# Kernel tuning notes

Measured on AMD Instinct MI355X. Metric: run time of the kernel, lower is better.

Reference implementation:

```python
import jax, jax.numpy as jnp
import numpy as np

HEADS = 8
DIM_HEAD = 64
NB_FEATURES = 256
DIM = 512

def setup_inputs() -> dict:
    key = jax.random.key(0)
    ks = jax.random.split(key, 4)
    b, n = 2, 8192
    x = jax.random.normal(ks[0], (b, n, DIM), jnp.float32)
    # fan-in scaling so exp(feature projections) stays numerically sane
    Wqkv = jax.random.normal(ks[1], (3 * HEADS * DIM_HEAD, DIM), jnp.float32) / np.sqrt(DIM).astype(np.float32)
    Wout = jax.random.normal(ks[2], (DIM, HEADS * DIM_HEAD), jnp.float32) / np.sqrt(HEADS * DIM_HEAD).astype(np.float32)
    bout = jnp.zeros((DIM,), jnp.float32)
    proj = jax.random.normal(ks[3], (NB_FEATURES, DIM_HEAD), jnp.float32) / np.sqrt(DIM_HEAD).astype(np.float32)
    return {"x": x, "Wqkv": Wqkv, "Wout": Wout, "bout": bout, "proj": proj}

def reference(x, Wqkv, Wout, bout, proj):
    b, n, _ = x.shape
    scale = DIM_HEAD ** -0.5
    qkv = jnp.einsum('bnd,ed->bne', x, Wqkv)            # [b,n,3*h*dh]
    q, k, v = jnp.split(qkv, 3, axis=-1)
    to_heads = lambda t: t.reshape(b, n, HEADS, DIM_HEAD).transpose(0, 2, 1, 3)  # [b,h,n,dh]
    q = to_heads(q) * scale
    k = to_heads(k)
    v = to_heads(v)
    # FAVOR+ exp feature maps
    q_prime = jnp.exp(jnp.einsum('bhnd,fd->bhnf', q, proj))  # [b,h,n,f]
    k_prime = jnp.exp(jnp.einsum('bhnd,fd->bhnf', k, proj))  # [b,h,n,f]
    k_sum = k_prime.sum(axis=2)                              # [b,h,f]
    D = jnp.einsum('bhnf,bhf->bhn', q_prime, k_sum)          # normalizer
    D_inv = 1.0 / (D + 1e-6)
    context = jnp.einsum('bhmf,bhmd->bhfd', k_prime, v)      # [b,h,f,dh]
    out = jnp.einsum('bhnf,bhfd->bhnd', q_prime, context) * D_inv[..., None]
    out = out.transpose(0, 2, 1, 3).reshape(b, n, HEADS * DIM_HEAD)
    return jnp.einsum('bne,de->bnd', out, Wout) + bout
```

## Files before the change

### kernel.cpp

```cpp
#include <hip/hip_runtime.h>
#include <math.h>

#define B_    2
#define NSEQ  8192
#define DIM_  512
#define H_    8
#define DH_   64
#define F_    256
#define M_    (B_*NSEQ)
#define QKV_  1536

typedef __attribute__((ext_vector_type(8))) short     short8;
typedef __attribute__((ext_vector_type(4))) float     float4v;
typedef __attribute__((ext_vector_type(8))) unsigned short ushort8v;

__device__ __forceinline__ unsigned short f2bf(float f) {
    unsigned u = __float_as_uint(f);
    u += 0x7FFFu + ((u >> 16) & 1u);
    return (unsigned short)(u >> 16);
}
__device__ __forceinline__ unsigned pack2bf(float lo, float hi) {
    return __builtin_amdgcn_perm(__float_as_uint(hi), __float_as_uint(lo), 0x07060302);
}
__device__ __forceinline__ void glds16(const void* g, void* s) {
    __builtin_amdgcn_global_load_lds(
        (const __attribute__((address_space(1))) unsigned int*)g,
        (__attribute__((address_space(3))) unsigned int*)s, 16, 0, 0);
}

__global__ __launch_bounds__(256) void cvt_bf16(const float* __restrict__ in,
                                                unsigned short* __restrict__ out,
                                                int n8) {
    int i = blockIdx.x * 256 + threadIdx.x;
    if (i >= n8) return;
    float4 a = ((const float4*)in)[2 * i];
    float4 b = ((const float4*)in)[2 * i + 1];
    ushort8v o;
    o[0] = f2bf(a.x); o[1] = f2bf(a.y); o[2] = f2bf(a.z); o[3] = f2bf(a.w);
    o[4] = f2bf(b.x); o[5] = f2bf(b.y); o[6] = f2bf(b.z); o[7] = f2bf(b.w);
    ((ushort8v*)out)[i] = o;
}

template<bool BF16OUT>
__global__ __launch_bounds__(256) void gemm_nt_mfma(const unsigned short* __restrict__ A,
                                                    const unsigned short* __restrict__ Bm,
                                                    const float* __restrict__ bias,
                                                    void* __restrict__ Cout,
                                                    int M, int N, int K) {
    __shared__ __align__(16) unsigned short As[128 * 32];
    __shared__ __align__(16) unsigned short Bs[128 * 32];
    const int t  = threadIdx.x;
    const int w  = t >> 6, l = t & 63;
    const int wm = w >> 1, wn = w & 1;
    const int m0 = blockIdx.y * 128, n0 = blockIdx.x * 128;
    const int lrow = l & 15, lkb = l >> 4;

    float4v acc[4][4];
#pragma unroll
    for (int mi = 0; mi < 4; mi++)
#pragma unroll
        for (int ni = 0; ni < 4; ni++) acc[mi][ni] = (float4v){0.f, 0.f, 0.f, 0.f};

    for (int k0 = 0; k0 < K; k0 += 32) {
        __syncthreads();
#pragma unroll
        for (int i = 0; i < 2; i++) {
            int rb8 = w * 2 + i;
            int row = rb8 * 16 + lrow;
            glds16(A + (size_t)(m0 + row) * K + k0 + lkb * 8, &As[rb8 * 512]);
            glds16(Bm + (size_t)(n0 + row) * K + k0 + lkb * 8, &Bs[rb8 * 512]);
        }
        __syncthreads();

        short8 af[4], bfr[4];
#pragma unroll
        for (int mi = 0; mi < 4; mi++)
            af[mi] = *(const short8*)&As[((wm * 4 + mi) * 64 + l) * 8];
#pragma unroll
        for (int ni = 0; ni < 4; ni++)
            bfr[ni] = *(const short8*)&Bs[((wn * 4 + ni) * 64 + l) * 8];
#pragma unroll
        for (int mi = 0; mi < 4; mi++)
#pragma unroll
            for (int ni = 0; ni < 4; ni++)
                acc[mi][ni] = __builtin_amdgcn_mfma_f32_16x16x32_bf16(
                    af[mi], bfr[ni], acc[mi][ni], 0, 0, 0);
    }

    const int q = l >> 4, c = l & 15;
#pragma unroll
    for (int mi = 0; mi < 4; mi++) {
        int row0 = m0 + wm * 64 + mi * 16 + q * 4;
#pragma unroll
        for (int ni = 0; ni < 4; ni++) {
            int col = n0 + wn * 64 + ni * 16 + c;
            float bv = bias ? bias[col] : 0.f;
#pragma unroll
            for (int r = 0; r < 4; r++) {
                float v = acc[mi][ni][r] + bv;
                if (BF16OUT) ((unsigned short*)Cout)[(size_t)(row0 + r) * N + col] = f2bf(v);
                else         ((float*)Cout)[(size_t)(row0 + r) * N + col] = v;
            }
        }
    }
}

__global__ __launch_bounds__(256) void vtrans(const unsigned short* __restrict__ qkvb,
                                              unsigned short* __restrict__ vT) {
    __shared__ unsigned short T[128][80];
    const int t = threadIdx.x;
    const int n0 = blockIdx.x * 128, z = blockIdx.y;
    const int b = z >> 3, h = z & 7;
#pragma unroll
    for (int i = 0; i < 4; i++) {
        int flat = t + i * 256;
        int n = flat >> 3, d8 = flat & 7;
        ushort8v v = *(const ushort8v*)(qkvb + ((size_t)b * NSEQ + n0 + n) * QKV_ + 1024 + h * 64 + d8 * 8);
        *(ushort8v*)&T[n][d8 * 8] = v;
    }
    __syncthreads();
#pragma unroll
    for (int i = 0; i < 4; i++) {
        int flat = t + i * 256;
        int d = flat >> 4, n8 = flat & 15;
        ushort8v o;
#pragma unroll
        for (int j = 0; j < 8; j++) o[j] = T[n8 * 8 + j][d];
        *(ushort8v*)(vT + ((size_t)z * 64 + d) * NSEQ + n0 + n8 * 8) = o;
    }
}

__global__ __launch_bounds__(256) void ctx_fused_mfma(
    const unsigned short* __restrict__ qkvb,
    const unsigned short* __restrict__ projb,
    const unsigned short* __restrict__ vT,
    float* __restrict__ partial)
{
    __shared__ __align__(16) unsigned short PB[32 * 512];
    __shared__ __align__(16) unsigned short KB[8 * 512];
    __shared__ __align__(16) unsigned short VB[8 * 512];
    __shared__ __align__(16) unsigned short KPA[32 * 512];
    const int t = threadIdx.x, w = t >> 6, l = t & 63;
    const int lr = l & 15, lq = l >> 4;
    const int s = blockIdx.x, z = blockIdx.y;
    const int b = z >> 3, h = z & 7;
    const int nchunk = s * 256;

    for (int idx = w; idx < 32; idx += 4) {
        int fblk = idx >> 1, kt = idx & 1;
        glds16(projb + (size_t)(fblk * 16 + lr) * 64 + kt * 32 + lq * 8, &PB[idx * 512]);
    }

    float4v acc[4][5];
#pragma unroll
    for (int mi = 0; mi < 4; mi++)
#pragma unroll
        for (int ni = 0; ni < 5; ni++) acc[mi][ni] = (float4v){0.f, 0.f, 0.f, 0.f};
    short ov = (lr == 0) ? (short)0x3F80 : (short)0;
    short8 ones = {ov, ov, ov, ov, ov, ov, ov, ov};

    for (int st = 0; st < 4; st++) {
        int nbase = nchunk + st * 64;
        __syncthreads();
        for (int idx = w; idx < 8; idx += 4) {
            int nblk = idx >> 1, kt = idx & 1;
            glds16(qkvb + ((size_t)b * NSEQ + nbase + nblk * 16 + lr) * QKV_ + 512 + h * 64 + kt * 32 + lq * 8,
                   &KB[idx * 512]);
        }
        for (int idx = w; idx < 8; idx += 4) {
            int dhb = idx >> 1, nt2 = idx & 1;
            glds16(vT + ((size_t)z * 64 + dhb * 16 + lr) * NSEQ + nbase + nt2 * 32 + lq * 8,
                   &VB[idx * 512]);
        }
        __syncthreads();

        float4v a2[4][4];
#pragma unroll
        for (int mi = 0; mi < 4; mi++)
#pragma unroll
            for (int ni = 0; ni < 4; ni++) a2[mi][ni] = (float4v){0.f, 0.f, 0.f, 0.f};
#pragma unroll
        for (int ks = 0; ks < 2; ks++) {
            short8 ka[4], pb[4];
#pragma unroll
            for (int mi = 0; mi < 4; mi++)
                ka[mi] = *(const short8*)&KB[((mi * 2 + ks) * 64 + l) * 8];
#pragma unroll
            for (int ni = 0; ni < 4; ni++)
                pb[ni] = *(const short8*)&PB[(((w * 4 + ni) * 2 + ks) * 64 + l) * 8];
#pragma unroll
            for (int mi = 0; mi < 4; mi++)
#pragma unroll
                for (int ni = 0; ni < 4; ni++)
                    a2[mi][ni] = __builtin_amdgcn_mfma_f32_16x16x32_bf16(ka[mi], pb[ni], a2[mi][ni], 0, 0, 0);
        }
#pragma unroll
        for (int mi = 0; mi < 4; mi++) {
            int nb = mi * 16 + lq * 4;
            int qoff = ((nb >> 3) & 3) * 256 + (nb & 7) * 2;
            int setn = nb >> 5;
#pragma unroll
            for (int ni = 0; ni < 4; ni++) {
                int f = w * 64 + ni * 16 + lr;
                float e0 = __expf(a2[mi][ni][0]);
                float e1 = __expf(a2[mi][ni][1]);
                float e2 = __expf(a2[mi][ni][2]);
                float e3 = __expf(a2[mi][ni][3]);
                uint2 p; p.x = pack2bf(e0, e1); p.y = pack2bf(e2, e3);
                *(uint2*)((char*)KPA + (size_t)(((f >> 4) * 2 + setn) * 1024 + qoff + (f & 15) * 16)) = p;
            }
        }
#pragma unroll
        for (int ks = 0; ks < 2; ks++) {
            short8 af[4], bf[4];
#pragma unroll
            for (int mi = 0; mi < 4; mi++)
                af[mi] = *(const short8*)&KPA[(((w * 4 + mi) * 2 + ks) * 64 + l) * 8];
#pragma unroll
            for (int ni = 0; ni < 4; ni++)
                bf[ni] = *(const short8*)&VB[((ni * 2 + ks) * 64 + l) * 8];
#pragma unroll
            for (int mi = 0; mi < 4; mi++) {
#pragma unroll
                for (int ni = 0; ni < 4; ni++)
                    acc[mi][ni] = __builtin_amdgcn_mfma_f32_16x16x32_bf16(af[mi], bf[ni], acc[mi][ni], 0, 0, 0);
                acc[mi][4] = __builtin_amdgcn_mfma_f32_16x16x32_bf16(af[mi], ones, acc[mi][4], 0, 0, 0);
            }
        }
    }
    float* base = partial + (size_t)(s * 16 + z) * 80 * 256;
#pragma unroll
    for (int mi = 0; mi < 4; mi++) {
        int f0r = w * 64 + mi * 16 + lq * 4;
#pragma unroll
        for (int ni = 0; ni < 5; ni++) {
            int col = ni * 16 + lr;
#pragma unroll
            for (int r = 0; r < 4; r++)
                base[(size_t)col * 256 + f0r + r] = acc[mi][ni][r];
        }
    }
}

__global__ __launch_bounds__(256) void ctx_reduce(const float* __restrict__ partial,
                                                  unsigned short* __restrict__ ctxT) {
    int idx = blockIdx.x * 256 + threadIdx.x;
    const int NC = 16 * 80 * 256;
    if (idx >= NC) return;
    float s = 0.f;
#pragma unroll
    for (int k = 0; k < 32; k++) s += partial[(size_t)k * NC + idx];
    ctxT[idx] = f2bf(s);
}

__global__ __launch_bounds__(256) void attn_fused_mfma(
    const unsigned short* __restrict__ qkvb,
    const unsigned short* __restrict__ projb,
    const unsigned short* __restrict__ ctxT,
    unsigned short* __restrict__ attnb)
{
    __shared__ __align__(16) unsigned short QB[16 * 512];
    __shared__ __align__(16) unsigned short PA[8 * 512];
    __shared__ __align__(16) unsigned short QPA[16 * 512];
    __shared__ __align__(16) unsigned short CB[10 * 512];
    const int t = threadIdx.x, w = t >> 6, l = t & 63;
    const int lr = l & 15, lq = l >> 4;
    const int m0 = blockIdx.x * 128, z = blockIdx.y;
    const int b = z >> 3, h = z & 7;

    for (int idx = w; idx < 16; idx += 4) {
        int mblk = idx >> 1, kt = idx & 1;
        glds16(qkvb + ((size_t)b * NSEQ + m0 + mblk * 16 + lr) * QKV_ + h * 64 + kt * 32 + lq * 8,
               &QB[idx * 512]);
    }
    float4v acc[2][5];
#pragma unroll
    for (int mi = 0; mi < 2; mi++)
#pragma unroll
        for (int ni = 0; ni < 5; ni++) acc[mi][ni] = (float4v){0.f, 0.f, 0.f, 0.f};

    for (int fs = 0; fs < 4; fs++) {
        int f0 = fs * 64;
        __syncthreads();
        for (int idx = w; idx < 8; idx += 4) {
            int fb = idx >> 1, kt = idx & 1;
            glds16(projb + (size_t)(f0 + fb * 16 + lr) * 64 + kt * 32 + lq * 8, &PA[idx * 512]);
        }
        for (int idx = w; idx < 10; idx += 4) {
            int dhb = idx >> 1, ft = idx & 1;
            glds16(ctxT + ((size_t)z * 80 + dhb * 16 + lr) * 256 + f0 + ft * 32 + lq * 8,
                   &CB[idx * 512]);
        }
        __syncthreads();

        float4v a2[4][2];
#pragma unroll
        for (int mi = 0; mi < 4; mi++)
#pragma unroll
            for (int ni = 0; ni < 2; ni++) a2[mi][ni] = (float4v){0.f, 0.f, 0.f, 0.f};
#pragma unroll
        for (int ks = 0; ks < 2; ks++) {
            short8 pa[4], qb[2];
#pragma unroll
            for (int mi = 0; mi < 4; mi++)
                pa[mi] = *(const short8*)&PA[((mi * 2 + ks) * 64 + l) * 8];
#pragma unroll
            for (int ni = 0; ni < 2; ni++)
                qb[ni] = *(const short8*)&QB[(((w * 2 + ni) * 2 + ks) * 64 + l) * 8];
#pragma unroll
            for (int mi = 0; mi < 4; mi++)
#pragma unroll
                for (int ni = 0; ni < 2; ni++)
                    a2[mi][ni] = __builtin_amdgcn_mfma_f32_16x16x32_bf16(pa[mi], qb[ni], a2[mi][ni], 0, 0, 0);
        }
#pragma unroll
        for (int mi = 0; mi < 4; mi++) {
            int fb2 = mi * 16 + lq * 4;
            int qoff = ((fb2 >> 3) & 3) * 256 + (fb2 & 7) * 2;
            int setf = fb2 >> 5;
#pragma unroll
            for (int ni = 0; ni < 2; ni++) {
                int m = w * 32 + ni * 16 + lr;
                float e0 = __expf(0.125f * a2[mi][ni][0]);
                float e1 = __expf(0.125f * a2[mi][ni][1]);
                float e2 = __expf(0.125f * a2[mi][ni][2]);
                float e3 = __expf(0.125f * a2[mi][ni][3]);
                uint2 p; p.x = pack2bf(e0, e1); p.y = pack2bf(e2, e3);
                *(uint2*)((char*)QPA + (size_t)(((m >> 4) * 2 + setf) * 1024 + qoff + (m & 15) * 16)) = p;
            }
        }
#pragma unroll
        for (int ks = 0; ks < 2; ks++) {
            short8 af[2], cb[5];
#pragma unroll
            for (int mi = 0; mi < 2; mi++)
                af[mi] = *(const short8*)&QPA[(((w * 2 + mi) * 2 + ks) * 64 + l) * 8];
#pragma unroll
            for (int ni = 0; ni < 5; ni++)
                cb[ni] = *(const short8*)&CB[((ni * 2 + ks) * 64 + l) * 8];
#pragma unroll
            for (int mi = 0; mi < 2; mi++)
#pragma unroll
                for (int ni = 0; ni < 5; ni++)
                    acc[mi][ni] = __builtin_amdgcn_mfma_f32_16x16x32_bf16(af[mi], cb[ni], acc[mi][ni], 0, 0, 0);
        }
    }
#pragma unroll
    for (int mi = 0; mi < 2; mi++) {
        int rowb = m0 + w * 32 + mi * 16 + lq * 4;
#pragma unroll
        for (int r = 0; r < 4; r++) {
            float dv = __shfl(acc[mi][4][r], (l & 48), 64);
            float rinv = 1.f / (dv + 1e-6f);
#pragma unroll
            for (int ni = 0; ni < 4; ni++)
                attnb[((size_t)b * NSEQ + rowb + r) * 512 + h * 64 + ni * 16 + lr] =
                    f2bf(acc[mi][ni][r] * rinv);
        }
    }
}

extern "C" void kernel_launch(void* const* d_in, const int* in_sizes, int n_in,
                              void* d_out, int out_size, void* d_ws, size_t ws_size,
                              hipStream_t stream) {
    const float* x    = (const float*)d_in[0];
    const float* Wqkv = (const float*)d_in[1];
    const float* Wout = (const float*)d_in[2];
    const float* bout = (const float*)d_in[3];
    const float* proj = (const float*)d_in[4];

    unsigned short* qkvb  = (unsigned short*)d_ws;
    unsigned short* vT    = qkvb + (size_t)M_ * QKV_;
    float*          partial = (float*)(vT + (size_t)16 * 64 * NSEQ);
    unsigned short* ctxT  = (unsigned short*)(partial + (size_t)32 * 16 * 80 * 256);
    unsigned short* projb = ctxT + (size_t)16 * 80 * 256;
    unsigned short* xb    = projb + 16384;
    unsigned short* attnb = xb;
    unsigned short* wqkvb = xb + (size_t)M_ * DIM_;
    unsigned short* woutb = wqkvb + (size_t)QKV_ * DIM_;
    float* outp = (float*)d_out;

    cvt_bf16<<<dim3(4096), 256, 0, stream>>>(x, xb, M_ * DIM_ / 8);
    cvt_bf16<<<dim3(384), 256, 0, stream>>>(Wqkv, wqkvb, QKV_ * DIM_ / 8);
    cvt_bf16<<<dim3(128), 256, 0, stream>>>(Wout, woutb, DIM_ * DIM_ / 8);
    cvt_bf16<<<dim3(8), 256, 0, stream>>>(proj, projb, F_ * DH_ / 8);
    gemm_nt_mfma<true><<<dim3(QKV_ / 128, M_ / 128), 256, 0, stream>>>(xb, wqkvb, nullptr, qkvb, M_, QKV_, DIM_);
    vtrans<<<dim3(64, 16), 256, 0, stream>>>(qkvb, vT);
    ctx_fused_mfma<<<dim3(32, 16), 256, 0, stream>>>(qkvb, projb, vT, partial);
    ctx_reduce<<<dim3(1280), 256, 0, stream>>>(partial, ctxT);
    attn_fused_mfma<<<dim3(64, 16), 256, 0, stream>>>(qkvb, projb, ctxT, attnb);
    gemm_nt_mfma<false><<<dim3(DIM_ / 128, M_ / 128), 256, 0, stream>>>(attnb, woutb, bout, outp, M_, DIM_, DIM_);
}
```

Measured before the change: 235.0 us.

## Merge bf16 conversions into one launch and enlarge QKV GEMM tile

The four float-to-bf16 conversion launches are merged into a single kernel that picks its source tensor by block index, removing launch overhead. The QKV projection GEMM moves to a new kernel with a 256x128 output tile and a K-step of 64, using 8x4 MFMA accumulators per wave, to raise data reuse per LDS load and cut the number of K iterations. The larger tile raises register and LDS pressure and halves the grid along M, which may reduce occupancy.

Measured after the change: 232.3 us. About the same (-1.2%).

```diff
diff --git a/kernel.cpp b/kernel.cpp
--- a/kernel.cpp
+++ b/kernel.cpp
@@ -28,17 +28,98 @@
         (__attribute__((address_space(3))) unsigned int*)s, 16, 0, 0);
 }
 
-__global__ __launch_bounds__(256) void cvt_bf16(const float* __restrict__ in,
-                                                unsigned short* __restrict__ out,
-                                                int n8) {
-    int i = blockIdx.x * 256 + threadIdx.x;
-    if (i >= n8) return;
+__global__ __launch_bounds__(256) void cvt_all(const float* __restrict__ x,
+                                               const float* __restrict__ wqkv,
+                                               const float* __restrict__ wout,
+                                               const float* __restrict__ proj,
+                                               unsigned short* __restrict__ xb,
+                                               unsigned short* __restrict__ wqkvb,
+                                               unsigned short* __restrict__ woutb,
+                                               unsigned short* __restrict__ projb) {
+    int bid = blockIdx.x;
+    const float* in; unsigned short* out; int i;
+    if (bid < 4096)      { in = x;    out = xb;    i = bid * 256 + threadIdx.x; }
+    else if (bid < 4480) { in = wqkv; out = wqkvb; i = (bid - 4096) * 256 + threadIdx.x; }
+    else if (bid < 4608) { in = wout; out = woutb; i = (bid - 4480) * 256 + threadIdx.x; }
+    else                 { in = proj; out = projb; i = (bid - 4608) * 256 + threadIdx.x; }
     float4 a = ((const float4*)in)[2 * i];
     float4 b = ((const float4*)in)[2 * i + 1];
     ushort8v o;
     o[0] = f2bf(a.x); o[1] = f2bf(a.y); o[2] = f2bf(a.z); o[3] = f2bf(a.w);
     o[4] = f2bf(b.x); o[5] = f2bf(b.y); o[6] = f2bf(b.z); o[7] = f2bf(b.w);
     ((ushort8v*)out)[i] = o;
+}
+
+template<bool BF16OUT>
+__global__ __launch_bounds__(256, 2) void gemm_nt_v2(const unsigned short* __restrict__ A,
+                                                     const unsigned short* __restrict__ Bm,
+                                                     const float* __restrict__ bias,
+                                                     void* __restrict__ Cout,
+                                                     int M, int N, int K) {
+    __shared__ __align__(16) unsigned short As[256 * 64];
+    __shared__ __align__(16) unsigned short Bs[128 * 64];
+    const int t  = threadIdx.x;
+    const int w  = t >> 6, l = t & 63;
+    const int wm = w >> 1, wn = w & 1;
+    const int m0 = blockIdx.y * 256, n0 = blockIdx.x * 128;
+    const int lr = l & 15, lq = l >> 4;
+
+    float4v acc[8][4];
+#pragma unroll
+    for (int mi = 0; mi < 8; mi++)
+#pragma unroll
+        for (int ni = 0; ni < 4; ni++) acc[mi][ni] = (float4v){0.f, 0.f, 0.f, 0.f};
+
+    for (int k0 = 0; k0 < K; k0 += 64) {
+        __syncthreads();
+#pragma unroll
+        for (int ii = 0; ii < 12; ii++) {
+            int idx = w + ii * 4;
+            if (idx < 32) {
+                glds16(A + (size_t)(m0 + (idx >> 1) * 16 + lr) * K + k0 + (idx & 1) * 32 + lq * 8,
+                       &As[idx * 512]);
+            } else {
+                int j = idx - 32;
+                glds16(Bm + (size_t)(n0 + (j >> 1) * 16 + lr) * K + k0 + (j & 1) * 32 + lq * 8,
+                       &Bs[j * 512]);
+            }
+        }
+        __syncthreads();
+
+#pragma unroll
+        for (int ks = 0; ks < 2; ks++) {
+            short8 af[8], bfr[4];
+#pragma unroll
+            for (int mi = 0; mi < 8; mi++)
+                af[mi] = *(const short8*)&As[(((wm * 8 + mi) * 2 + ks) * 64 + l) * 8];
+#pragma unroll
+            for (int ni = 0; ni < 4; ni++)
+                bfr[ni] = *(const short8*)&Bs[(((wn * 4 + ni) * 2 + ks) * 64 + l) * 8];
+#pragma unroll
+            for (int mi = 0; mi < 8; mi++)
+#pragma unroll
+                for (int ni = 0; ni < 4; ni++)
+                    acc[mi][ni] = __builtin_amdgcn_mfma_f32_16x16x32_bf16(
+                        af[mi], bfr[ni], acc[mi][ni], 0, 0, 0);
+        }
+    }
+
+    const int q = l >> 4, c = l & 15;
+#pragma unroll
+    for (int mi = 0; mi < 8; mi++) {
+        int row0 = m0 + wm * 128 + mi * 16 + q * 4;
+#pragma unroll
+        for (int ni = 0; ni < 4; ni++) {
+            int col = n0 + wn * 64 + ni * 16 + c;
+            float bv = bias ? bias[col] : 0.f;
+#pragma unroll
+            for (int r = 0; r < 4; r++) {
+                float v = acc[mi][ni][r] + bv;
+                if (BF16OUT) ((unsigned short*)Cout)[(size_t)(row0 + r) * N + col] = f2bf(v);
+                else         ((float*)Cout)[(size_t)(row0 + r) * N + col] = v;
+            }
+        }
+    }
 }
 
 template<bool BF16OUT>
@@ -380,11 +461,8 @@
     unsigned short* woutb = wqkvb + (size_t)QKV_ * DIM_;
     float* outp = (float*)d_out;
 
-    cvt_bf16<<<dim3(4096), 256, 0, stream>>>(x, xb, M_ * DIM_ / 8);
-    cvt_bf16<<<dim3(384), 256, 0, stream>>>(Wqkv, wqkvb, QKV_ * DIM_ / 8);
-    cvt_bf16<<<dim3(128), 256, 0, stream>>>(Wout, woutb, DIM_ * DIM_ / 8);
-    cvt_bf16<<<dim3(8), 256, 0, stream>>>(proj, projb, F_ * DH_ / 8);
-    gemm_nt_mfma<true><<<dim3(QKV_ / 128, M_ / 128), 256, 0, stream>>>(xb, wqkvb, nullptr, qkvb, M_, QKV_, DIM_);
+    cvt_all<<<dim3(4616), 256, 0, stream>>>(x, Wqkv, Wout, proj, xb, wqkvb, woutb, projb);
+    gemm_nt_v2<true><<<dim3(QKV_ / 128, M_ / 256), 256, 0, stream>>>(xb, wqkvb, nullptr, qkvb, M_, QKV_, DIM_);
     vtrans<<<dim3(64, 16), 256, 0, stream>>>(qkvb, vT);
     ctx_fused_mfma<<<dim3(32, 16), 256, 0, stream>>>(qkvb, projb, vT, partial);
     ctx_reduce<<<dim3(1280), 256, 0, stream>>>(partial, ctxT);
```

## Double-buffer GEMM LDS staging and merge bf16 conversion launches

Applied to the files above, without the earlier changes.

The NT GEMM now uses two LDS buffers, so the global-to-LDS load for the next K tile is issued before the MFMAs on the current tile, with one barrier per iteration instead of two. The four separate fp32-to-bf16 conversion launches are merged into one kernel that picks its source by block index, cutting launch overhead. Double buffering doubles GEMM LDS use to 32KB per block, which may lower occupancy.

Measured after the change: 229.7 us. 2.2% less time.

```diff
diff --git a/kernel.cpp b/kernel.cpp
--- a/kernel.cpp
+++ b/kernel.cpp
@@ -28,11 +28,20 @@
         (__attribute__((address_space(3))) unsigned int*)s, 16, 0, 0);
 }
 
-__global__ __launch_bounds__(256) void cvt_bf16(const float* __restrict__ in,
-                                                unsigned short* __restrict__ out,
-                                                int n8) {
-    int i = blockIdx.x * 256 + threadIdx.x;
-    if (i >= n8) return;
+__global__ __launch_bounds__(256) void cvt_all(const float* __restrict__ x,
+                                               const float* __restrict__ wqkv,
+                                               const float* __restrict__ wout,
+                                               const float* __restrict__ proj,
+                                               unsigned short* __restrict__ xb,
+                                               unsigned short* __restrict__ wqkvb,
+                                               unsigned short* __restrict__ woutb,
+                                               unsigned short* __restrict__ projb) {
+    int bid = blockIdx.x;
+    const float* in; unsigned short* out; int i;
+    if (bid < 4096)      { in = x;    out = xb;    i = bid * 256 + threadIdx.x; }
+    else if (bid < 4480) { in = wqkv; out = wqkvb; i = (bid - 4096) * 256 + threadIdx.x; }
+    else if (bid < 4608) { in = wout; out = woutb; i = (bid - 4480) * 256 + threadIdx.x; }
+    else                 { in = proj; out = projb; i = (bid - 4608) * 256 + threadIdx.x; }
     float4 a = ((const float4*)in)[2 * i];
     float4 b = ((const float4*)in)[2 * i + 1];
     ushort8v o;
@@ -42,18 +51,18 @@
 }
 
 template<bool BF16OUT>
-__global__ __launch_bounds__(256) void gemm_nt_mfma(const unsigned short* __restrict__ A,
-                                                    const unsigned short* __restrict__ Bm,
-                                                    const float* __restrict__ bias,
-                                                    void* __restrict__ Cout,
-                                                    int M, int N, int K) {
-    __shared__ __align__(16) unsigned short As[128 * 32];
-    __shared__ __align__(16) unsigned short Bs[128 * 32];
+__global__ __launch_bounds__(256) void gemm_nt_pp(const unsigned short* __restrict__ A,
+                                                  const unsigned short* __restrict__ Bm,
+                                                  const float* __restrict__ bias,
+                                                  void* __restrict__ Cout,
+                                                  int M, int N, int K) {
+    __shared__ __align__(16) unsigned short As[2][128 * 32];
+    __shared__ __align__(16) unsigned short Bs[2][128 * 32];
     const int t  = threadIdx.x;
     const int w  = t >> 6, l = t & 63;
     const int wm = w >> 1, wn = w & 1;
     const int m0 = blockIdx.y * 128, n0 = blockIdx.x * 128;
-    const int lrow = l & 15, lkb = l >> 4;
+    const int lr = l & 15, lq = l >> 4;
 
     float4v acc[4][4];
 #pragma unroll
@@ -61,30 +70,39 @@
 #pragma unroll
         for (int ni = 0; ni < 4; ni++) acc[mi][ni] = (float4v){0.f, 0.f, 0.f, 0.f};
 
-    for (int k0 = 0; k0 < K; k0 += 32) {
-        __syncthreads();
+    auto stage = [&](int buf, int k0) {
 #pragma unroll
         for (int i = 0; i < 2; i++) {
             int rb8 = w * 2 + i;
-            int row = rb8 * 16 + lrow;
-            glds16(A + (size_t)(m0 + row) * K + k0 + lkb * 8, &As[rb8 * 512]);
-            glds16(Bm + (size_t)(n0 + row) * K + k0 + lkb * 8, &Bs[rb8 * 512]);
-        }
-        __syncthreads();
+            int row = rb8 * 16 + lr;
+            glds16(A + (size_t)(m0 + row) * K + k0 + lq * 8, &As[buf][rb8 * 512]);
+            glds16(Bm + (size_t)(n0 + row) * K + k0 + lq * 8, &Bs[buf][rb8 * 512]);
+        }
+    };
+
+    const int nk = K >> 5;
+    stage(0, 0);
+    __syncthreads();
+
+    for (int k = 0; k < nk; k++) {
+        const int cur = k & 1;
+        if (k + 1 < nk) stage(cur ^ 1, (k + 1) << 5);
 
         short8 af[4], bfr[4];
 #pragma unroll
         for (int mi = 0; mi < 4; mi++)
-            af[mi] = *(const short8*)&As[((wm * 4 + mi) * 64 + l) * 8];
+            af[mi] = *(const short8*)&As[cur][((wm * 4 + mi) * 64 + l) * 8];
 #pragma unroll
         for (int ni = 0; ni < 4; ni++)
-            bfr[ni] = *(const short8*)&Bs[((wn * 4 + ni) * 64 + l) * 8];
+            bfr[ni] = *(const short8*)&Bs[cur][((wn * 4 + ni) * 64 + l) * 8];
 #pragma unroll
         for (int mi = 0; mi < 4; mi++)
 #pragma unroll
             for (int ni = 0; ni < 4; ni++)
                 acc[mi][ni] = __builtin_amdgcn_mfma_f32_16x16x32_bf16(
                     af[mi], bfr[ni], acc[mi][ni], 0, 0, 0);
+
+        if (k + 1 < nk) __syncthreads();
     }
 
     const int q = l >> 4, c = l & 15;
@@ -380,14 +398,11 @@
     unsigned short* woutb = wqkvb + (size_t)QKV_ * DIM_;
     float* outp = (float*)d_out;
 
-    cvt_bf16<<<dim3(4096), 256, 0, stream>>>(x, xb, M_ * DIM_ / 8);
-    cvt_bf16<<<dim3(384), 256, 0, stream>>>(Wqkv, wqkvb, QKV_ * DIM_ / 8);
-    cvt_bf16<<<dim3(128), 256, 0, stream>>>(Wout, woutb, DIM_ * DIM_ / 8);
-    cvt_bf16<<<dim3(8), 256, 0, stream>>>(proj, projb, F_ * DH_ / 8);
-    gemm_nt_mfma<true><<<dim3(QKV_ / 128, M_ / 128), 256, 0, stream>>>(xb, wqkvb, nullptr, qkvb, M_, QKV_, DIM_);
+    cvt_all<<<dim3(4616), 256, 0, stream>>>(x, Wqkv, Wout, proj, xb, wqkvb, woutb, projb);
+    gemm_nt_pp<true><<<dim3(QKV_ / 128, M_ / 128), 256, 0, stream>>>(xb, wqkvb, nullptr, qkvb, M_, QKV_, DIM_);
     vtrans<<<dim3(64, 16), 256, 0, stream>>>(qkvb, vT);
     ctx_fused_mfma<<<dim3(32, 16), 256, 0, stream>>>(qkvb, projb, vT, partial);
     ctx_reduce<<<dim3(1280), 256, 0, stream>>>(partial, ctxT);
     attn_fused_mfma<<<dim3(64, 16), 256, 0, stream>>>(qkvb, projb, ctxT, attnb);
-    gemm_nt_mfma<false><<<dim3(DIM_ / 128, M_ / 128), 256, 0, stream>>>(attnb, woutb, bout, outp, M_, DIM_, DIM_);
-}
+    gemm_nt_pp<false><<<dim3(DIM_ / 128, M_ / 128), 256, 0, stream>>>(attnb, woutb, bout, outp, M_, DIM_, DIM_);
+}
```
